# Optimization experiments

Hardware: AMD Instinct MI355X
Metric: run time of the kernel (lower is better)

The kernel has to match this reference:

```python
import jax, jax.numpy as jnp
import numpy as np

B, S, HID = 2, 2048, 1024
NH, NKV, HD = 16, 4, 64
MAXPOS, THETA, EPS = 4096, 10000.0, 1e-6


def _rope_tables():
    inv_freq = 1.0 / (THETA ** (jnp.arange(0, HD, 2, dtype=jnp.float32) / HD))
    t = jnp.arange(MAXPOS, dtype=jnp.float32)
    freqs = jnp.outer(t, inv_freq)                      # [MAXPOS, HD/2]
    emb = jnp.concatenate([freqs, freqs], axis=-1)      # [MAXPOS, HD]
    return jnp.cos(emb), jnp.sin(emb)


def setup_inputs() -> dict:
    key = jax.random.key(0)
    ks = jax.random.split(key, 8)
    cos, sin = _rope_tables()
    neg = jnp.finfo(jnp.float32).min
    causal = jnp.where(jnp.tril(jnp.ones((S, S), dtype=bool)), 0.0, neg)
    sc = 0.02
    return {
        "hidden_states": jax.random.normal(ks[0], (B, S, HID), jnp.float32),
        "cos": cos,
        "sin": sin,
        "position_ids": jnp.broadcast_to(jnp.arange(S, dtype=jnp.int32), (B, S)),
        "attention_mask": causal[None, None, :, :],
        "Wq": jax.random.normal(ks[1], (NH * HD, HID), jnp.float32) * sc,
        "Wk": jax.random.normal(ks[2], (NKV * HD, HID), jnp.float32) * sc,
        "Wv": jax.random.normal(ks[3], (NKV * HD, HID), jnp.float32) * sc,
        "Wo": jax.random.normal(ks[4], (HID, NH * HD), jnp.float32) * sc,
        "q_norm_w": jnp.ones((HD,), jnp.float32),
        "k_norm_w": jnp.ones((HD,), jnp.float32),
    }


def _rms_norm(x, w):
    xf = x.astype(jnp.float32)
    var = jnp.mean(xf * xf, axis=-1, keepdims=True)
    return (w * (xf * jax.lax.rsqrt(var + EPS))).astype(x.dtype)


def _rotate_half(x):
    x1, x2 = jnp.split(x, 2, axis=-1)
    return jnp.concatenate([-x2, x1], axis=-1)


def reference(hidden_states, cos, sin, position_ids, attention_mask,
              Wq, Wk, Wv, Wo, q_norm_w, k_norm_w):
    b, s, _ = hidden_states.shape
    # projections -> [b, heads, s, hd]
    q = (hidden_states @ Wq.T).reshape(b, s, NH, HD).transpose(0, 2, 1, 3)
    k = (hidden_states @ Wk.T).reshape(b, s, NKV, HD).transpose(0, 2, 1, 3)
    v = (hidden_states @ Wv.T).reshape(b, s, NKV, HD).transpose(0, 2, 1, 3)
    # per-head RMS norm on head_dim
    q = _rms_norm(q, q_norm_w)
    k = _rms_norm(k, k_norm_w)
    # rotary embedding (unsqueeze_dim=1 -> broadcast over heads)
    c = cos[position_ids][:, None, :, :]  # [b,1,s,hd]
    sn = sin[position_ids][:, None, :, :]
    q = q * c + _rotate_half(q) * sn
    k = k * c + _rotate_half(k) * sn
    # GQA: repeat kv heads
    n_rep = NH // NKV
    k = jnp.repeat(k, n_rep, axis=1)
    v = jnp.repeat(v, n_rep, axis=1)
    # attention
    scores = jnp.einsum("bhqd,bhkd->bhqk", q, k) / np.sqrt(HD).astype(np.float32)
    scores = scores + attention_mask
    probs = jax.nn.softmax(scores.astype(jnp.float32), axis=-1).astype(q.dtype)
    ctx = jnp.einsum("bhqk,bhkd->bhqd", probs, v)  # [b,NH,s,hd]
    ctx = ctx.transpose(0, 2, 1, 3).reshape(b, s, NH * HD)
    return ctx @ Wo.T
```

## Files before the change

kernel.cpp:

```cpp
#include <hip/hip_runtime.h>
#include <stdint.h>

#define S_LEN 2048
#define HIDDEN 1024
#define NH 16
#define NKV 4
#define HD 64

typedef unsigned short u16;
typedef __attribute__((ext_vector_type(8))) short short8;
typedef __attribute__((ext_vector_type(4))) float f32x4;
typedef __attribute__((ext_vector_type(16))) float f32x16;
typedef __attribute__((ext_vector_type(4))) uint32_t u32x4;

__device__ __forceinline__ u16 f2b(float f) {
  uint32_t u = __float_as_uint(f);
  uint32_t r = u + 0x7fffu + ((u >> 16) & 1u);
  return (u16)(r >> 16);
}
__device__ __forceinline__ float b2f(u16 b) {
  return __uint_as_float(((uint32_t)b) << 16);
}
__device__ __forceinline__ void gll16(const void* g, void* l) {
  __builtin_amdgcn_global_load_lds(
      (const __attribute__((address_space(1))) uint32_t*)g,
      (__attribute__((address_space(3))) uint32_t*)l, 16, 0, 0);
}

__global__ __launch_bounds__(256) void f2b_multi(
    const float* __restrict__ s0, u16* __restrict__ d0, int n0,
    const float* __restrict__ s1, u16* __restrict__ d1, int n1,
    const float* __restrict__ s2, u16* __restrict__ d2, int n2,
    const float* __restrict__ s3, u16* __restrict__ d3, int n3,
    const float* __restrict__ s4, u16* __restrict__ d4, int n4) {
  int i = blockIdx.x * 256 + threadIdx.x;
  const float* s;
  u16* d;
  int idx = i;
  if (i < n0) { s = s0; d = d0; }
  else if ((idx = i - n0) < n1) { s = s1; d = d1; }
  else if ((idx = i - n0 - n1) < n2) { s = s2; d = d2; }
  else if ((idx = i - n0 - n1 - n2) < n3) { s = s3; d = d3; }
  else if ((idx = i - n0 - n1 - n2 - n3) < n4) { s = s4; d = d4; }
  else return;
  f32x4 a = *reinterpret_cast<const f32x4*>(&s[(size_t)idx * 8]);
  f32x4 b = *reinterpret_cast<const f32x4*>(&s[(size_t)idx * 8 + 4]);
  short8 t;
#pragma unroll
  for (int k = 0; k < 4; ++k) t[k] = (short)f2b(a[k]);
#pragma unroll
  for (int k = 0; k < 4; ++k) t[4 + k] = (short)f2b(b[k]);
  *reinterpret_cast<short8*>(&d[(size_t)idx * 8]) = t;
}

template <int OUT_BF16>
__global__ __launch_bounds__(512) void gemm_bt(const u16* __restrict__ A,
                                               const u16* __restrict__ B,
                                               void* __restrict__ Cv,
                                               int M, int N, int K) {
  __shared__ u16 As[128][64];
  __shared__ u16 Bs[128][64];
  const int tid = threadIdx.x;
  const int wid = tid >> 6, lane = tid & 63;
  const int fr = lane & 15, fg = lane >> 4;
  const int m0 = blockIdx.x * 128, n0 = blockIdx.y * 128;
  const int wr = wid >> 2, wc = wid & 3;
  const int srow = lane >> 3, scol = (lane & 7) << 3;
  f32x4 acc[4][2] = {};

  for (int k0 = 0; k0 < K; k0 += 64) {
    __syncthreads();
#pragma unroll
    for (int i = 0; i < 2; ++i) {
      const int c = wid + i * 8;
      gll16(&A[(size_t)(m0 + c * 8 + srow) * K + k0 + scol], &As[c * 8][0]);
      gll16(&B[(size_t)(n0 + c * 8 + srow) * K + k0 + scol], &Bs[c * 8][0]);
    }
    __syncthreads();
#pragma unroll
    for (int ks = 0; ks < 2; ++ks) {
      short8 a[4], b[2];
#pragma unroll
      for (int i = 0; i < 4; ++i)
        a[i] = *reinterpret_cast<const short8*>(
            &As[wr * 64 + i * 16 + fr][ks * 32 + fg * 8]);
#pragma unroll
      for (int j = 0; j < 2; ++j)
        b[j] = *reinterpret_cast<const short8*>(
            &Bs[wc * 32 + j * 16 + fr][ks * 32 + fg * 8]);
#pragma unroll
      for (int i = 0; i < 4; ++i)
#pragma unroll
        for (int j = 0; j < 2; ++j)
          acc[i][j] = __builtin_amdgcn_mfma_f32_16x16x32_bf16(a[i], b[j], acc[i][j], 0, 0, 0);
    }
  }

  const int rb = fg * 4;
#pragma unroll
  for (int i = 0; i < 4; ++i)
#pragma unroll
    for (int j = 0; j < 2; ++j) {
      const int row0 = m0 + wr * 64 + i * 16 + rb;
      const int col = n0 + wc * 32 + j * 16 + fr;
#pragma unroll
      for (int r = 0; r < 4; ++r) {
        size_t idx = (size_t)(row0 + r) * N + col;
        if (OUT_BF16) ((u16*)Cv)[idx] = f2b(acc[i][j][r]);
        else          ((float*)Cv)[idx] = acc[i][j][r];
      }
    }
}

__global__ __launch_bounds__(256) void normrope(const u16* __restrict__ qkv,
                                                const int* __restrict__ pos_ids,
                                                const float* __restrict__ cosT,
                                                const float* __restrict__ sinT,
                                                const float* __restrict__ qw,
                                                const float* __restrict__ kw,
                                                u16* __restrict__ Qn,
                                                u16* __restrict__ Kn) {
  const int w = blockIdx.x * 4 + (threadIdx.x >> 6);
  const int lane = threadIdx.x & 63;
  const int row = w / 20, unit = w % 20;
  const int b = row >> 11, s = row & 2047;
  float x = b2f(qkv[(size_t)row * 1536 + unit * 64 + lane]);
  const bool isq = unit < 16;
  const int h = isq ? unit : unit - 16;
  float ss = x * x;
  ss += __shfl_xor(ss, 1);
  ss += __shfl_xor(ss, 2);
  ss += __shfl_xor(ss, 4);
  ss += __shfl_xor(ss, 8);
  ss += __shfl_xor(ss, 16);
  ss += __shfl_xor(ss, 32);
  float r = rsqrtf(ss * (1.0f / 64.0f) + 1e-6f);
  float xn = x * r * (isq ? qw[lane] * 0.18033688011112042f : kw[lane]);
  const int p = pos_ids[row];
  const float c = cosT[p * 64 + lane];
  const float sn = sinT[p * 64 + lane];
  float partner = __shfl_xor(xn, 32);
  float out = xn * c + (lane < 32 ? -partner : partner) * sn;
  if (isq) Qn[((size_t)(b * NH + h) * S_LEN + s) * HD + lane] = f2b(out);
  else     Kn[((size_t)(b * NKV + h) * S_LEN + s) * HD + lane] = f2b(out);
}

__global__ __launch_bounds__(256) void vtrans(const u16* __restrict__ qkv,
                                              u16* __restrict__ Vt) {
  const int s0 = blockIdx.x * 64;
  const int b = blockIdx.y >> 2, hv = blockIdx.y & 3;
  __shared__ u16 t[64][72];
  const int tid = threadIdx.x;
  const int r = tid >> 2, cq = (tid & 3) << 4;
#pragma unroll
  for (int i = 0; i < 2; ++i)
    *reinterpret_cast<short8*>(&t[r][cq + i * 8]) =
        *reinterpret_cast<const short8*>(
            &qkv[(size_t)(b * S_LEN + s0 + r) * 1536 + 1280 + hv * 64 + cq + i * 8]);
  __syncthreads();
  const int d = tid >> 2, sq = (tid & 3) << 4;
#pragma unroll
  for (int i = 0; i < 2; ++i) {
    u16 tmp[8];
#pragma unroll
    for (int k = 0; k < 8; ++k) tmp[k] = t[sq + i * 8 + k][d];
    *reinterpret_cast<short8*>(
        &Vt[((size_t)(b * NKV + hv) * HD + d) * S_LEN + s0 + sq + i * 8]) =
        *reinterpret_cast<short8*>(tmp);
  }
}

__device__ __forceinline__ void attn_tile(const u16* __restrict__ K,
                                          const u16* __restrict__ V,
                                          const short8 qf[4], int kv0, bool domask,
                                          int col, int hi,
                                          f32x16& o0, f32x16& o1, float& m, float& l) {
  short8 v0 = *reinterpret_cast<const short8*>(&V[(size_t)col * S_LEN + kv0 + hi * 8]);
  short8 v1 = *reinterpret_cast<const short8*>(&V[(size_t)col * S_LEN + kv0 + 16 + hi * 8]);
  short8 v2 = *reinterpret_cast<const short8*>(&V[(size_t)(32 + col) * S_LEN + kv0 + hi * 8]);
  short8 v3 = *reinterpret_cast<const short8*>(&V[(size_t)(32 + col) * S_LEN + kv0 + 16 + hi * 8]);
  f32x16 sA = {}, sB = {};
  {
    short8 k0 = *reinterpret_cast<const short8*>(&K[(size_t)(kv0 + col) * HD + hi * 8]);
    short8 k1 = *reinterpret_cast<const short8*>(&K[(size_t)(kv0 + col) * HD + 16 + hi * 8]);
    short8 k2 = *reinterpret_cast<const short8*>(&K[(size_t)(kv0 + col) * HD + 32 + hi * 8]);
    short8 k3 = *reinterpret_cast<const short8*>(&K[(size_t)(kv0 + col) * HD + 48 + hi * 8]);
    sA = __builtin_amdgcn_mfma_f32_32x32x16_bf16(k0, qf[0], sA, 0, 0, 0);
    sB = __builtin_amdgcn_mfma_f32_32x32x16_bf16(k1, qf[1], sB, 0, 0, 0);
    sA = __builtin_amdgcn_mfma_f32_32x32x16_bf16(k2, qf[2], sA, 0, 0, 0);
    sB = __builtin_amdgcn_mfma_f32_32x32x16_bf16(k3, qf[3], sB, 0, 0, 0);
  }
  f32x16 s = sA + sB;
  if (domask) {
#pragma unroll
    for (int r = 0; r < 16; ++r) {
      int kvr = (r & 3) + 8 * (r >> 2) + 4 * hi;
      s[r] = (kvr <= col) ? s[r] : -3.0e38f;
    }
  }
  float t8[8];
#pragma unroll
  for (int r = 0; r < 8; ++r) t8[r] = fmaxf(s[r], s[r + 8]);
#pragma unroll
  for (int r = 0; r < 4; ++r) t8[r] = fmaxf(t8[r], t8[r + 4]);
  float tm = fmaxf(fmaxf(t8[0], t8[1]), fmaxf(t8[2], t8[3]));
  tm = fmaxf(tm, __shfl_xor(tm, 32));
  if (!__all(tm <= m + 8.0f)) {
    float mn = fmaxf(m, tm);
    float al = exp2f(m - mn);
    m = mn;
    l *= al;
#pragma unroll
    for (int r = 0; r < 16; ++r) { o0[r] *= al; o1[r] *= al; }
  }
  float p[16];
#pragma unroll
  for (int r = 0; r < 16; ++r) p[r] = exp2f(s[r] - m);
  float u8[8];
#pragma unroll
  for (int r = 0; r < 8; ++r) u8[r] = p[r] + p[r + 8];
#pragma unroll
  for (int r = 0; r < 4; ++r) u8[r] += u8[r + 4];
  float ps = (u8[0] + u8[1]) + (u8[2] + u8[3]);
  ps += __shfl_xor(ps, 32);
  l += ps;
  uint32_t w[8], x[8];
#pragma unroll
  for (int i = 0; i < 8; ++i) {
    uint32_t wo;
    asm("v_cvt_pk_bf16_f32 %0, %1, %2" : "=v"(wo) : "v"(p[2 * i]), "v"(p[2 * i + 1]));
    w[i] = wo;
  }
#pragma unroll
  for (int i = 0; i < 8; ++i) x[i] = (uint32_t)__shfl_xor((int)w[i], 32);
  u32x4 bw0 = {hi ? x[2] : w[0], hi ? x[3] : w[1], hi ? w[2] : x[0], hi ? w[3] : x[1]};
  u32x4 bw1 = {hi ? x[6] : w[4], hi ? x[7] : w[5], hi ? w[6] : x[4], hi ? w[7] : x[5]};
  short8 B0 = __builtin_bit_cast(short8, bw0);
  short8 B1 = __builtin_bit_cast(short8, bw1);
  o0 = __builtin_amdgcn_mfma_f32_32x32x16_bf16(v0, B0, o0, 0, 0, 0);
  o0 = __builtin_amdgcn_mfma_f32_32x32x16_bf16(v1, B1, o0, 0, 0, 0);
  o1 = __builtin_amdgcn_mfma_f32_32x32x16_bf16(v2, B0, o1, 0, 0, 0);
  o1 = __builtin_amdgcn_mfma_f32_32x32x16_bf16(v3, B1, o1, 0, 0, 0);
}

__global__ __launch_bounds__(256) void attn_kernel(const u16* __restrict__ Qn,
                                                   const u16* __restrict__ Kn,
                                                   const u16* __restrict__ Vt,
                                                   u16* __restrict__ ctx) {
  const int bh = blockIdx.y;
  const int b = bh >> 4, h = bh & 15, hkv = h >> 2;
  const u16* Q = Qn + (size_t)bh * S_LEN * HD;
  const u16* K = Kn + (size_t)(b * NKV + hkv) * S_LEN * HD;
  const u16* V = Vt + (size_t)(b * NKV + hkv) * HD * S_LEN;
  const int wid = threadIdx.x >> 6, lane = threadIdx.x & 63;
  const int col = lane & 31, hi = lane >> 5;
  const int j = blockIdx.x;
  int qt;
  if (wid == 0) qt = j;
  else if (wid == 1) qt = 31 - j;
  else if (wid == 2) qt = 32 + j;
  else qt = 63 - j;
  const int q0 = qt * 32;

  short8 qf[4];
#pragma unroll
  for (int d = 0; d < 4; ++d)
    qf[d] = *reinterpret_cast<const short8*>(&Q[(size_t)(q0 + col) * HD + d * 16 + hi * 8]);

  f32x16 oA0 = {}, oA1 = {}, oB0 = {}, oB1 = {};
  float mA = -3.0e38f, lA = 0.0f, mB = -3.0e38f, lB = 0.0f;

  int kt = 0;
  for (; kt + 1 <= qt; kt += 2) {
    attn_tile(K, V, qf, kt * 32, false, col, hi, oA0, oA1, mA, lA);
    attn_tile(K, V, qf, (kt + 1) * 32, kt + 1 == qt, col, hi, oB0, oB1, mB, lB);
  }
  if (kt <= qt)
    attn_tile(K, V, qf, kt * 32, kt == qt, col, hi, oA0, oA1, mA, lA);

  float M = fmaxf(mA, mB);
  float wA = exp2f(mA - M), wB = exp2f(mB - M);
  float l = wA * lA + wB * lB;
  const float invl = 1.0f / l;
  __shared__ __align__(16) u16 Tl[4][32][72];
#pragma unroll
  for (int r = 0; r < 16; ++r) {
    int dl = (r & 3) + 8 * (r >> 2) + 4 * hi;
    Tl[wid][col][dl] = f2b((wA * oA0[r] + wB * oB0[r]) * invl);
    Tl[wid][col][32 + dl] = f2b((wA * oA1[r] + wB * oB1[r]) * invl);
  }
#pragma unroll
  for (int k2 = 0; k2 < 4; ++k2) {
    short8 vv = *reinterpret_cast<const short8*>(&Tl[wid][col][hi * 32 + k2 * 8]);
    *reinterpret_cast<short8*>(
        &ctx[((size_t)(b * S_LEN) + q0 + col) * (NH * HD) + h * HD + hi * 32 + k2 * 8]) = vv;
  }
}

extern "C" void kernel_launch(void* const* d_in, const int* in_sizes, int n_in,
                              void* d_out, int out_size, void* d_ws, size_t ws_size,
                              hipStream_t stream) {
  const float* hidden = (const float*)d_in[0];
  const float* cosT   = (const float*)d_in[1];
  const float* sinT   = (const float*)d_in[2];
  const int*   pos    = (const int*)d_in[3];
  const float* Wq = (const float*)d_in[5];
  const float* Wk = (const float*)d_in[6];
  const float* Wv = (const float*)d_in[7];
  const float* Wo = (const float*)d_in[8];
  const float* qw = (const float*)d_in[9];
  const float* kw = (const float*)d_in[10];

  char* p = (char*)d_ws;
  u16* hb   = (u16*)p; p += (size_t)4096 * 1024 * 2;
  u16* wqkv = (u16*)p; p += (size_t)1536 * 1024 * 2;
  u16* wob  = (u16*)p; p += (size_t)1024 * 1024 * 2;
  u16* qkvr = (u16*)p; p += (size_t)4096 * 1536 * 2;
  u16* qn   = (u16*)p; p += (size_t)(NH * 2) * S_LEN * HD * 2;
  u16* kn   = (u16*)p; p += (size_t)(NKV * 2) * S_LEN * HD * 2;
  u16* vt   = (u16*)p; p += (size_t)(NKV * 2) * HD * S_LEN * 2;
  u16* ctx  = (u16*)p; p += (size_t)4096 * 1024 * 2;

  f2b_multi<<<3332, 256, 0, stream>>>(hidden, hb, 524288,
                                      Wq, wqkv, 131072,
                                      Wk, wqkv + 1048576, 32768,
                                      Wv, wqkv + 1310720, 32768,
                                      Wo, wob, 131072);

  gemm_bt<1><<<dim3(32, 12), 512, 0, stream>>>(hb, wqkv, qkvr, 4096, 1536, 1024);

  normrope<<<20480, 256, 0, stream>>>(qkvr, pos, cosT, sinT, qw, kw, qn, kn);
  vtrans<<<dim3(32, 8), 256, 0, stream>>>(qkvr, vt);

  attn_kernel<<<dim3(16, 2 * NH), 256, 0, stream>>>(qn, kn, vt, ctx);

  gemm_bt<0><<<dim3(32, 8), 512, 0, stream>>>(ctx, wob, d_out, 4096, 1024, 1024);
}
```

Measured before the change: 247.5 us.

## Split each query tile's KV loop across two waves and merge via LDS

Each block now handles two query tiles, each shared by a pair of waves. The two waves in a pair take alternating KV tiles and their online-softmax partial states are combined through shared memory. The grid doubles to 32x32 blocks. This shortens the per-wave serial dependency chain and adds more waves for latency hiding. In exchange it adds an LDS round-trip, a block-wide barrier, half the waves sitting idle during the epilogue, and more shared memory per block.

Measured after the change: 256.1 us. 3.5% more time.

```diff
diff --git a/kernel.cpp b/kernel.cpp
--- a/kernel.cpp
+++ b/kernel.cpp
@@ -255,43 +255,53 @@
   const int wid = threadIdx.x >> 6, lane = threadIdx.x & 63;
   const int col = lane & 31, hi = lane >> 5;
   const int j = blockIdx.x;
-  int qt;
-  if (wid == 0) qt = j;
-  else if (wid == 1) qt = 31 - j;
-  else if (wid == 2) qt = 32 + j;
-  else qt = 63 - j;
+  const int pair = wid >> 1, par = wid & 1;
+  const int qt = pair ? j : 63 - j;
   const int q0 = qt * 32;
+
+  __shared__ float Pm[2][32], Pl[2][32];
+  __shared__ float Po[2][32][65];
+  __shared__ __align__(16) u16 Tl[2][32][72];
 
   short8 qf[4];
 #pragma unroll
   for (int d = 0; d < 4; ++d)
     qf[d] = *reinterpret_cast<const short8*>(&Q[(size_t)(q0 + col) * HD + d * 16 + hi * 8]);
 
-  f32x16 oA0 = {}, oA1 = {}, oB0 = {}, oB1 = {};
-  float mA = -3.0e38f, lA = 0.0f, mB = -3.0e38f, lB = 0.0f;
-
-  int kt = 0;
-  for (; kt + 1 <= qt; kt += 2) {
-    attn_tile(K, V, qf, kt * 32, false, col, hi, oA0, oA1, mA, lA);
-    attn_tile(K, V, qf, (kt + 1) * 32, kt + 1 == qt, col, hi, oB0, oB1, mB, lB);
-  }
-  if (kt <= qt)
-    attn_tile(K, V, qf, kt * 32, kt == qt, col, hi, oA0, oA1, mA, lA);
-
-  float M = fmaxf(mA, mB);
-  float wA = exp2f(mA - M), wB = exp2f(mB - M);
-  float l = wA * lA + wB * lB;
-  const float invl = 1.0f / l;
-  __shared__ __align__(16) u16 Tl[4][32][72];
+  f32x16 o0 = {}, o1 = {};
+  float m = -3.0e38f, l = 0.0f;
+
+  for (int kt = par; kt <= qt; kt += 2)
+    attn_tile(K, V, qf, kt * 32, kt == qt, col, hi, o0, o1, m, l);
+
+  if (par) {
+    if (hi == 0) { Pm[pair][col] = m; Pl[pair][col] = l; }
+#pragma unroll
+    for (int r = 0; r < 16; ++r) {
+      int dl = (r & 3) + 8 * (r >> 2) + 4 * hi;
+      Po[pair][col][dl] = o0[r];
+      Po[pair][col][32 + dl] = o1[r];
+    }
+  }
+  __syncthreads();
+  if (par) return;
+
+  float m1 = Pm[pair][col], l1 = Pl[pair][col];
+  float M = fmaxf(m, m1);
+  float w0 = exp2f(m - M), w1 = exp2f(m1 - M);
+  float L = w0 * l + w1 * l1;
+  const float invL = 1.0f / L;
 #pragma unroll
   for (int r = 0; r < 16; ++r) {
     int dl = (r & 3) + 8 * (r >> 2) + 4 * hi;
-    Tl[wid][col][dl] = f2b((wA * oA0[r] + wB * oB0[r]) * invl);
-    Tl[wid][col][32 + dl] = f2b((wA * oA1[r] + wB * oB1[r]) * invl);
+    float a0 = w0 * o0[r] + w1 * Po[pair][col][dl];
+    float a1 = w0 * o1[r] + w1 * Po[pair][col][32 + dl];
+    Tl[pair][col][dl] = f2b(a0 * invL);
+    Tl[pair][col][32 + dl] = f2b(a1 * invL);
   }
 #pragma unroll
   for (int k2 = 0; k2 < 4; ++k2) {
-    short8 vv = *reinterpret_cast<const short8*>(&Tl[wid][col][hi * 32 + k2 * 8]);
+    short8 vv = *reinterpret_cast<const short8*>(&Tl[pair][col][hi * 32 + k2 * 8]);
     *reinterpret_cast<short8*>(
         &ctx[((size_t)(b * S_LEN) + q0 + col) * (NH * HD) + h * HD + hi * 32 + k2 * 8]) = vv;
   }
@@ -332,7 +342,7 @@
   normrope<<<20480, 256, 0, stream>>>(qkvr, pos, cosT, sinT, qw, kw, qn, kn);
   vtrans<<<dim3(32, 8), 256, 0, stream>>>(qkvr, vt);
 
-  attn_kernel<<<dim3(16, 2 * NH), 256, 0, stream>>>(qn, kn, vt, ctx);
+  attn_kernel<<<dim3(32, 2 * NH), 256, 0, stream>>>(qn, kn, vt, ctx);
 
   gemm_bt<0><<<dim3(32, 8), 512, 0, stream>>>(ctx, wob, d_out, 4096, 1024, 1024);
 }
```
